# Kernel tuning notes

Hardware: AMD Instinct MI355X
Metric: run time of the kernel (lower is better)

The kernel has to match this reference:

```python
import jax, jax.numpy as jnp
import numpy as np

DOWNSAMPLING_K = 64  # number of pooled key/value positions


def setup_inputs() -> dict:
    key = jax.random.key(0)
    ks = jax.random.split(key, 8)
    B, S, H, N, D = 4, 4096, 1024, 16, 64
    s_in = 0.02  # glorot-like scale for H=1024 fan-in
    return {
        "query": jax.random.normal(ks[0], (B, S, H), jnp.float32),
        "key": jax.random.normal(ks[1], (B, S, H), jnp.float32),
        "value": jax.random.normal(ks[2], (B, S, H), jnp.float32),
        "Wq": jax.random.normal(ks[3], (H, N, D), jnp.float32) * s_in,
        "bq": jnp.zeros((N, D), jnp.float32),
        "Wk": jax.random.normal(ks[4], (H, N, D), jnp.float32) * s_in,
        "bk": jnp.zeros((N, D), jnp.float32),
        "Wv": jax.random.normal(ks[5], (H, N, D), jnp.float32) * s_in,
        "bv": jnp.zeros((N, D), jnp.float32),
        "Wo": jax.random.normal(ks[6], (N, D, H), jnp.float32) * s_in,
        "bo": jnp.zeros((H,), jnp.float32),
        "step": 0,
        "train": 0,
    }


def _downsample(x, k):
    # x: [B, S, N, D] -> mean-pool along sequence into k buckets -> [B, k, N, D]
    B, S, N, D = x.shape
    return x.reshape(B, k, S // k, N, D).mean(axis=2)


def reference(query, key, value, Wq, bq, Wk, bk, Wv, bv, Wo, bo, step, train):
    # QKV projections (DenseGeneral features=(num_heads, head_dim))
    q = jnp.einsum("bsh,hnd->bsnd", query, Wq) + bq  # [B,S,N,D]
    k = jnp.einsum("bsh,hnd->bsnd", key, Wk) + bk
    v = jnp.einsum("bsh,hnd->bsnd", value, Wv) + bv
    # Downsampled (sparse) attention: pool K,V to DOWNSAMPLING_K positions
    kd = _downsample(k, DOWNSAMPLING_K)  # [B,K,N,D]
    vd = _downsample(v, DOWNSAMPLING_K)
    scale = 1.0 / jnp.sqrt(jnp.asarray(q.shape[-1], q.dtype))
    scores = jnp.einsum("bsnd,bknd->bnsk", q, kd) * scale  # [B,N,S,K]
    attn = jax.nn.softmax(scores, axis=-1)
    a_v = jnp.einsum("bnsk,bknd->bsnd", attn, vd)  # [B,S,N,D]
    # Output projection (DenseGeneral over (-2,-1))
    out = jnp.einsum("bsnd,ndh->bsh", a_v, Wo) + bo  # [B,S,H]
    return out
```

## Files before the change

### kernel.cpp

```cpp
#include <hip/hip_runtime.h>

typedef unsigned short u16;
typedef unsigned int u32;
typedef __attribute__((ext_vector_type(8))) short bf16x8_t;
typedef __attribute__((ext_vector_type(4))) float f32x4_t;


#define MFMA_BF16 __builtin_amdgcn_mfma_f32_16x16x32_bf16

__device__ __forceinline__ u16 f2bf(float f) {
  union { float f; u32 u; } a; a.f = f;
  u32 u = a.u;
  u32 r = (u + 0x7FFFu + ((u >> 16) & 1u)) >> 16;
  return (u16)r;
}

__device__ __forceinline__ void async_load16(const void* g, void* l) {
  __builtin_amdgcn_global_load_lds(
      (const __attribute__((address_space(1))) void*)g,
      (__attribute__((address_space(3))) void*)l, 16, 0, 0);
}

__device__ __forceinline__ void stage64(const u16* __restrict__ src,
                                        char* lds_base, int t) {
  const int r = t >> 3;
  const int gch = (t & 7) ^ (r & 7);
  async_load16(src + (size_t)r * 1024 + gch * 8, lds_base + (t >> 6) * 1024);
}

__device__ __forceinline__ void acc4(float4& a, const float4 b) {
  a.x += b.x; a.y += b.y; a.z += b.z; a.w += b.w;
}

__global__ __launch_bounds__(512) void fused_stream(
    const float* __restrict__ query, const float* __restrict__ key,
    const float* __restrict__ value, const float* __restrict__ W0,
    const float* __restrict__ W1, const float* __restrict__ W2,
    const float* __restrict__ W3, u16* __restrict__ qcvt, u16* __restrict__ keyd,
    u16* __restrict__ valued, u16* __restrict__ T0, u16* __restrict__ T1,
    u16* __restrict__ T2, u16* __restrict__ T3) {
  __shared__ char smem[32768];
  const int z = blockIdx.x;
  const int t = threadIdx.x;
  if (z < 512) {
    float (*part)[256][4] = (float(*)[256][4])smem;
    const int bkk = z & 255;
    const float* x = (z >= 256) ? value : key;
    u16* xd = (z >= 256) ? valued : keyd;
    const int lane = t & 63, w = t >> 6;
    const float* base = x + (size_t)bkk * 65536 + (size_t)w * 8 * 1024;
#define LD4(j, s) (*(const float4*)(base + (size_t)(j) * 1024 + ((s) * 64 + lane) * 4))
    float4 a0 = {0.f, 0.f, 0.f, 0.f}, a1 = a0, a2 = a0, a3 = a0;
    float4 u0 = LD4(0, 0), u1 = LD4(0, 1), u2 = LD4(0, 2), u3 = LD4(0, 3);
    float4 u4 = LD4(1, 0), u5 = LD4(1, 1), u6 = LD4(1, 2), u7 = LD4(1, 3);
    float4 v0 = LD4(2, 0), v1 = LD4(2, 1), v2 = LD4(2, 2), v3 = LD4(2, 3);
    float4 v4 = LD4(3, 0), v5 = LD4(3, 1), v6 = LD4(3, 2), v7 = LD4(3, 3);
    acc4(a0, u0); acc4(a1, u1); acc4(a2, u2); acc4(a3, u3);
    acc4(a0, u4); acc4(a1, u5); acc4(a2, u6); acc4(a3, u7);
    u0 = LD4(4, 0); u1 = LD4(4, 1); u2 = LD4(4, 2); u3 = LD4(4, 3);
    u4 = LD4(5, 0); u5 = LD4(5, 1); u6 = LD4(5, 2); u7 = LD4(5, 3);
    acc4(a0, v0); acc4(a1, v1); acc4(a2, v2); acc4(a3, v3);
    acc4(a0, v4); acc4(a1, v5); acc4(a2, v6); acc4(a3, v7);
    v0 = LD4(6, 0); v1 = LD4(6, 1); v2 = LD4(6, 2); v3 = LD4(6, 3);
    v4 = LD4(7, 0); v5 = LD4(7, 1); v6 = LD4(7, 2); v7 = LD4(7, 3);
    acc4(a0, u0); acc4(a1, u1); acc4(a2, u2); acc4(a3, u3);
    acc4(a0, u4); acc4(a1, u5); acc4(a2, u6); acc4(a3, u7);
    acc4(a0, v0); acc4(a1, v1); acc4(a2, v2); acc4(a3, v3);
    acc4(a0, v4); acc4(a1, v5); acc4(a2, v6); acc4(a3, v7);
#undef LD4
    *(float4*)&part[w][0 * 64 + lane][0] = a0;
    *(float4*)&part[w][1 * 64 + lane][0] = a1;
    *(float4*)&part[w][2 * 64 + lane][0] = a2;
    *(float4*)&part[w][3 * 64 + lane][0] = a3;
    __syncthreads();
    if (t < 256) {
      float4 s = {0.f, 0.f, 0.f, 0.f};
#pragma unroll
      for (int w2 = 0; w2 < 8; ++w2) {
        const float4 v = *(const float4*)&part[w2][t][0];
        s.x += v.x; s.y += v.y; s.z += v.z; s.w += v.w;
      }
      ushort4 r;
      r.x = f2bf(s.x * 0.015625f);
      r.y = f2bf(s.y * 0.015625f);
      r.z = f2bf(s.z * 0.015625f);
      r.w = f2bf(s.w * 0.015625f);
      *(ushort4*)(xd + (size_t)bkk * 1024 + t * 4) = r;
    }
  } else if (z < 4608) {
    const size_t i = ((size_t)(z - 512) * 512 + t) * 8;
    const float4 a = *(const float4*)(query + i);
    const float4 b = *(const float4*)(query + i + 4);
    bf16x8_t o;
    o[0] = (short)f2bf(a.x); o[1] = (short)f2bf(a.y);
    o[2] = (short)f2bf(a.z); o[3] = (short)f2bf(a.w);
    o[4] = (short)f2bf(b.x); o[5] = (short)f2bf(b.y);
    o[6] = (short)f2bf(b.z); o[7] = (short)f2bf(b.w);
    *(bf16x8_t*)(qcvt + i) = o;
  } else {
    float (*tile)[65] = (float(*)[65])smem;
    const int blk = z - 4608;
    const int wsel = blk >> 8, tidx = blk & 255;
    const float* W = (wsel == 0) ? W0 : (wsel == 1) ? W1 : (wsel == 2) ? W2 : W3;
    u16* WT = (wsel == 0) ? T0 : (wsel == 1) ? T1 : (wsel == 2) ? T2 : T3;
    const int tr = (tidx >> 4) * 64;
    const int tc = (tidx & 15) * 64;
#pragma unroll
    for (int i = 0; i < 8; ++i) {
      int idx = i * 512 + t;
      int r = idx >> 6, c = idx & 63;
      tile[r][c] = W[(size_t)(tr + r) * 1024 + tc + c];
    }
    __syncthreads();
#pragma unroll
    for (int i = 0; i < 8; ++i) {
      int idx = i * 512 + t;
      int r = idx >> 6, c = idx & 63;
      WT[(size_t)(tc + r) * 1024 + tr + c] = f2bf(tile[c][r]);
    }
  }
}

__global__ __launch_bounds__(256) void gemm_kv(const u16* __restrict__ A0,
                                               const u16* __restrict__ A1,
                                               const u16* __restrict__ BT0,
                                               const u16* __restrict__ BT1,
                                               const float* __restrict__ bias0,
                                               const float* __restrict__ bias1,
                                               u16* __restrict__ C0,
                                               u16* __restrict__ C1) {
  constexpr int K = 1024, BK = 32;
  __shared__ u16 sA[128 * BK];
  __shared__ u16 sB[128 * BK];
  const int z = blockIdx.z;
  const u16* A = z ? A1 : A0;
  const u16* BT = z ? BT1 : BT0;
  const float* bias = z ? bias1 : bias0;
  u16* Cv = z ? C1 : C0;
  const int t = threadIdx.x;
  const int lane = t & 63;
  const int w = t >> 6;
  const int wr = w >> 1, wc = w & 1;
  const int m0 = blockIdx.x * 128;
  const int n0 = blockIdx.y * 128;
  const int c16 = lane & 15, r16 = lane >> 4;

  f32x4_t acc[4][4] = {};

  for (int k0 = 0; k0 < K; k0 += BK) {
#pragma unroll
    for (int i = 0; i < 2; ++i) {
      const int idx = i * 256 + t;
      const int row = idx >> 2, ch = idx & 3;
      const int gch = ch ^ ((row >> 1) & 3);
      async_load16(A + (size_t)(m0 + row) * K + k0 + gch * 8,
                   (char*)sA + (i * 256 + w * 64) * 16);
    }
#pragma unroll
    for (int i = 0; i < 2; ++i) {
      const int idx = i * 256 + t;
      const int row = idx >> 2, ch = idx & 3;
      const int gch = ch ^ ((row >> 1) & 3);
      async_load16(BT + (size_t)(n0 + row) * K + k0 + gch * 8,
                   (char*)sB + (i * 256 + w * 64) * 16);
    }
    __syncthreads();

    bf16x8_t af[4], bfv[4];
#pragma unroll
    for (int m = 0; m < 4; ++m) {
      const int ra = wr * 64 + m * 16 + c16;
      af[m] = *(const bf16x8_t*)&sA[ra * BK + ((r16 ^ ((ra >> 1) & 3)) << 3)];
    }
#pragma unroll
    for (int n = 0; n < 4; ++n) {
      const int rb = wc * 64 + n * 16 + c16;
      bfv[n] = *(const bf16x8_t*)&sB[rb * BK + ((r16 ^ ((rb >> 1) & 3)) << 3)];
    }
#pragma unroll
    for (int m = 0; m < 4; ++m)
#pragma unroll
      for (int n = 0; n < 4; ++n)
        acc[m][n] = MFMA_BF16(af[m], bfv[n], acc[m][n], 0, 0, 0);
    __syncthreads();
  }

#pragma unroll
  for (int m = 0; m < 4; ++m) {
    const int row0 = m0 + wr * 64 + m * 16 + r16 * 4;
#pragma unroll
    for (int n = 0; n < 4; ++n) {
      const int col = n0 + wc * 64 + n * 16 + c16;
      const float bvl = bias[col];
#pragma unroll
      for (int i = 0; i < 4; ++i) {
        const float val = acc[m][n][i] + bvl;
        if (z)
          Cv[(size_t)col * 256 + row0 + i] = f2bf(val);
        else
          Cv[(size_t)(row0 + i) * 1024 + col] = f2bf(val);
      }
    }
  }
}

#define GEMM256_KLOOP(A_, BT_)                                                          \
  const u16* Ab = (A_) + (size_t)bx * 256 * 1024;                                       \
  const u16* Bb = (BT_) + (size_t)by * 256 * 1024;                                      \
  stage64(Ab,                   lds,                 t);                                \
  stage64(Ab + 128 * 1024,      lds + 128 * 128,     t);                                \
  stage64(Bb,                   lds + 32768,         t);                                \
  stage64(Bb + 64 * 1024,       lds + 32768 + 8192,  t);                                \
  stage64(Bb + 128 * 1024,      lds + 32768 + 16384, t);                                \
  stage64(Bb + 192 * 1024,      lds + 32768 + 24576, t);                                \
  stage64(Ab + 64 * 1024,       lds + 64 * 128,      t);                                \
  stage64(Ab + 192 * 1024,      lds + 192 * 128,     t);                                \
  stage64(Ab + 64,              lds + 65536,         t);                                \
  stage64(Ab + 128 * 1024 + 64, lds + 65536 + 16384, t);                                \
  stage64(Bb + 64,              lds + 98304,         t);                                \
  stage64(Bb + 64 * 1024 + 64,  lds + 98304 + 8192,  t);                                \
  stage64(Bb + 128 * 1024 + 64, lds + 98304 + 16384, t);                                \
  stage64(Bb + 192 * 1024 + 64, lds + 98304 + 24576, t);                                \
  asm volatile("s_waitcnt vmcnt(6)" ::: "memory");                                      \
  __builtin_amdgcn_s_barrier();                                                         \
  for (int kt = 0; kt < 16; ++kt) {                                                     \
    const int slot = kt & 1;                                                            \
    const u16* sAs = (const u16*)(lds + slot * 65536);                                  \
    const u16* sBs = (const u16*)(lds + slot * 65536 + 32768);                          \
    char* sAn = lds + (slot ^ 1) * 65536;                                               \
    char* sAc = lds + slot * 65536;                                                     \
    char* sBc = lds + slot * 65536 + 32768;                                             \
    const int k1 = (kt < 15 ? kt + 1 : 15) * 64;                                        \
    const int k2 = (kt < 14 ? kt + 2 : 15) * 64;                                        \
    bf16x8_t af[4][2];                                                                  \
    _Pragma("unroll") for (int m = 0; m < 4; ++m) {                                     \
      const int row = wm * 128 + m * 16 + c16;                                          \
      _Pragma("unroll") for (int kk = 0; kk < 2; ++kk)                                  \
        af[m][kk] = *(const bf16x8_t*)&sAs[row * 64 + (((kk * 4 + r16) ^ c7) << 3)];    \
    }                                                                                   \
    _Pragma("unroll") for (int n = 0; n < 2; ++n) {                                     \
      const int row = wn * 64 + n * 16 + c16;                                           \
      _Pragma("unroll") for (int kk = 0; kk < 2; ++kk)                                  \
        bfr[n][kk] = *(const bf16x8_t*)&sBs[row * 64 + (((kk * 4 + r16) ^ c7) << 3)];   \
    }                                                                                   \
    stage64(Ab + (size_t)64 * 1024 + k1,  sAn + 64 * 128,  t);                          \
    stage64(Ab + (size_t)192 * 1024 + k1, sAn + 192 * 128, t);                          \
    asm volatile("" ::: "memory");                                                      \
    __builtin_amdgcn_s_barrier();                                                       \
    asm volatile("s_waitcnt lgkmcnt(0)" ::: "memory");                                  \
    __builtin_amdgcn_sched_barrier(0);                                                  \
    __builtin_amdgcn_s_setprio(1);                                                      \
    _Pragma("unroll") for (int m = 0; m < 4; ++m)                                       \
      _Pragma("unroll") for (int n = 0; n < 2; ++n)                                     \
        _Pragma("unroll") for (int kk = 0; kk < 2; ++kk)                                \
          acc[m][n] = MFMA_BF16(af[m][kk], bfr[n][kk], acc[m][n], 0, 0, 0);             \
    __builtin_amdgcn_s_setprio(0);                                                      \
    asm volatile("" ::: "memory");                                                      \
    __builtin_amdgcn_s_barrier();                                                       \
    _Pragma("unroll") for (int n = 2; n < 4; ++n) {                                     \
      const int row = wn * 64 + n * 16 + c16;                                           \
      _Pragma("unroll") for (int kk = 0; kk < 2; ++kk)                                  \
        bfr[n][kk] = *(const bf16x8_t*)&sBs[row * 64 + (((kk * 4 + r16) ^ c7) << 3)];   \
    }                                                                                   \
    stage64(Ab + k2,                      sAc,             t);                          \
    stage64(Ab + (size_t)128 * 1024 + k2, sAc + 128 * 128, t);                          \
    asm volatile("" ::: "memory");                                                      \
    __builtin_amdgcn_s_barrier();                                                       \
    asm volatile("s_waitcnt lgkmcnt(0)" ::: "memory");                                  \
    __builtin_amdgcn_sched_barrier(0);                                                  \
    __builtin_amdgcn_s_setprio(1);                                                      \
    _Pragma("unroll") for (int m = 0; m < 4; ++m)                                       \
      _Pragma("unroll") for (int n = 2; n < 4; ++n)                                     \
        _Pragma("unroll") for (int kk = 0; kk < 2; ++kk)                                \
          acc[m][n] = MFMA_BF16(af[m][kk], bfr[n][kk], acc[m][n], 0, 0, 0);             \
    __builtin_amdgcn_s_setprio(0);                                                      \
    asm volatile("s_waitcnt vmcnt(10)" ::: "memory");                                   \
    __builtin_amdgcn_s_barrier();                                                       \
    _Pragma("unroll") for (int m = 0; m < 4; ++m) {                                     \
      const int row = wm * 128 + 64 + m * 16 + c16;                                     \
      _Pragma("unroll") for (int kk = 0; kk < 2; ++kk)                                  \
        af[m][kk] = *(const bf16x8_t*)&sAs[row * 64 + (((kk * 4 + r16) ^ c7) << 3)];    \
    }                                                                                   \
    stage64(Bb + k2,                     sBc,        t);                                \
    stage64(Bb + (size_t)64 * 1024 + k2, sBc + 8192, t);                                \
    asm volatile("" ::: "memory");                                                      \
    __builtin_amdgcn_s_barrier();                                                       \
    asm volatile("s_waitcnt lgkmcnt(0)" ::: "memory");                                  \
    __builtin_amdgcn_sched_barrier(0);                                                  \
    __builtin_amdgcn_s_setprio(1);                                                      \
    _Pragma("unroll") for (int m = 0; m < 4; ++m)                                       \
      _Pragma("unroll") for (int n = 0; n < 2; ++n)                                     \
        _Pragma("unroll") for (int kk = 0; kk < 2; ++kk)                                \
          acc[4 + m][n] = MFMA_BF16(af[m][kk], bfr[n][kk], acc[4 + m][n], 0, 0, 0);     \
    __builtin_amdgcn_s_setprio(0);                                                      \
    asm volatile("" ::: "memory");                                                      \
    __builtin_amdgcn_s_barrier();                                                       \
    stage64(Bb + (size_t)128 * 1024 + k2, sBc + 16384, t);                              \
    stage64(Bb + (size_t)192 * 1024 + k2, sBc + 24576, t);                              \
    asm volatile("" ::: "memory");                                                      \
    __builtin_amdgcn_s_barrier();                                                       \
    __builtin_amdgcn_sched_barrier(0);                                                  \
    __builtin_amdgcn_s_setprio(1);                                                      \
    _Pragma("unroll") for (int m = 0; m < 4; ++m)                                       \
      _Pragma("unroll") for (int n = 2; n < 4; ++n)                                     \
        _Pragma("unroll") for (int kk = 0; kk < 2; ++kk)                                \
          acc[4 + m][n] = MFMA_BF16(af[m][kk], bfr[n][kk], acc[4 + m][n], 0, 0, 0);     \
    __builtin_amdgcn_s_setprio(0);                                                      \
    asm volatile("s_waitcnt vmcnt(8)" ::: "memory");                                    \
    __builtin_amdgcn_s_barrier();                                                       \
  }

template <bool C_BF16>
__global__ __launch_bounds__(512) void gemm256(const u16* __restrict__ A,
                                               const u16* __restrict__ BT,
                                               const float* __restrict__ bias,
                                               void* __restrict__ Cv) {
  __shared__ u16 sAB[65536];
  char* lds = (char*)sAB;
  const int t = threadIdx.x;
  const int lane = t & 63;
  const int w = t >> 6;
  const int wm = w >> 2, wn = w & 3;
  const int c16 = lane & 15, r16 = lane >> 4, c7 = c16 & 7;
  const int tile = (blockIdx.x & 7) * 32 + (blockIdx.x >> 3);
  const int bx = tile >> 2, by = tile & 3;
  f32x4_t acc[8][4] = {};
  bf16x8_t bfr[4][2];
  GEMM256_KLOOP(A, BT)
#pragma unroll
  for (int m = 0; m < 8; ++m) {
    const int grow = bx * 256 + wm * 128 + m * 16 + r16 * 4;
#pragma unroll
    for (int n = 0; n < 4; ++n) {
      const int col = by * 256 + wn * 64 + n * 16 + c16;
      const float bvl = bias[col];
#pragma unroll
      for (int i = 0; i < 4; ++i) {
        const float val = acc[m][n][i] + bvl;
        if constexpr (C_BF16)
          ((u16*)Cv)[(size_t)(grow + i) * 1024 + col] = f2bf(val);
        else
          ((float*)Cv)[(size_t)(grow + i) * 1024 + col] = val;
      }
    }
  }
}

#define ATTN_EPI_HALF(HALF)                                                              \
  {                                                                                      \
    asm volatile("s_waitcnt lgkmcnt(0)" ::: "memory");                                   \
    _Pragma("unroll") for (int m = 0; m < 4; ++m)                                        \
      _Pragma("unroll") for (int nq = 0; nq < 4; ++nq) {                                 \
        const int d = nq * 16 + c16;                                                     \
        const float bvl = bias[n_head * 64 + d];                                         \
        _Pragma("unroll") for (int i = 0; i < 4; ++i) {                                  \
          const int row = m * 16 + r16 * 4 + i;                                          \
          qh[(row * 128 + ((d * 2) ^ ((row & 7) << 4))) >> 1] =                          \
              f2bf(acc[HALF * 4 + m][nq][i] + bvl);                                      \
        }                                                                                \
      }                                                                                  \
    if (HALF == 0) {                                                                     \
      asm volatile("s_waitcnt vmcnt(0) lgkmcnt(0)" ::: "memory");                        \
      __builtin_amdgcn_s_barrier();                                                      \
    } else {                                                                             \
      asm volatile("s_waitcnt lgkmcnt(0)" ::: "memory");                                 \
    }                                                                                    \
    bf16x8_t aq[4][2];                                                                   \
    _Pragma("unroll") for (int st = 0; st < 4; ++st) {                                   \
      const int row = st * 16 + c16;                                                     \
      const int rsw = (row & 7) << 4;                                                    \
      _Pragma("unroll") for (int dt = 0; dt < 2; ++dt)                                   \
        aq[st][dt] =                                                                     \
            *(const bf16x8_t*)&qh[(row * 128 + ((dt * 64 + r16 * 16) ^ rsw)) >> 1];      \
    }                                                                                    \
    asm volatile("s_waitcnt lgkmcnt(0)" ::: "memory");                                   \
    __builtin_amdgcn_sched_barrier(0);                                                   \
    u16* sP = qh;                                                                        \
    _Pragma("unroll") for (int st = 0; st < 4; ++st) {                                   \
      f32x4_t accs[4];                                                                   \
      _Pragma("unroll") for (int nn = 0; nn < 4; ++nn) {                                 \
        const u16* kr = &kdw[(nn * 16 + c16) * 64];                                      \
        bf16x8_t b0 = *(const bf16x8_t*)&kr[((r16 * 16) ^ swz) >> 1];                    \
        bf16x8_t b1 = *(const bf16x8_t*)&kr[((64 + r16 * 16) ^ swz) >> 1];               \
        f32x4_t a = {0.f, 0.f, 0.f, 0.f};                                                \
        a = MFMA_BF16(aq[st][0], b0, a, 0, 0, 0);                                        \
        a = MFMA_BF16(aq[st][1], b1, a, 0, 0, 0);                                        \
        accs[nn] = a;                                                                    \
      }                                                                                  \
      float ex[4][4], rs[4];                                                             \
      _Pragma("unroll") for (int i = 0; i < 4; ++i) {                                    \
        float mx = fmaxf(fmaxf(accs[0][i], accs[1][i]), fmaxf(accs[2][i], accs[3][i]));  \
        _Pragma("unroll") for (int off = 1; off < 16; off <<= 1)                         \
          mx = fmaxf(mx, __shfl_xor(mx, off));                                           \
        mx *= 0.125f;                                                                    \
        float s = 0.f;                                                                   \
        _Pragma("unroll") for (int nn = 0; nn < 4; ++nn) {                               \
          float e = __expf(accs[nn][i] * 0.125f - mx);                                   \
          ex[nn][i] = e;                                                                 \
          s += e;                                                                        \
        }                                                                                \
        _Pragma("unroll") for (int off = 1; off < 16; off <<= 1)                         \
          s += __shfl_xor(s, off);                                                       \
        rs[i] = 1.f / s;                                                                 \
      }                                                                                  \
      _Pragma("unroll") for (int i = 0; i < 4; ++i) {                                    \
        const int row = r16 * 4 + i;                                                     \
        const int rsw = (row & 7) << 4;                                                  \
        _Pragma("unroll") for (int nn = 0; nn < 4; ++nn)                                 \
          sP[row * 64 + (((nn * 32 + c16 * 2) ^ rsw) >> 1)] = f2bf(ex[nn][i]);           \
      }                                                                                  \
      asm volatile("s_waitcnt lgkmcnt(0)" ::: "memory");                                 \
      bf16x8_t pa0 = *(const bf16x8_t*)&sP[c16 * 64 + (((r16 * 16) ^ swz) >> 1)];        \
      bf16x8_t pa1 = *(const bf16x8_t*)&sP[c16 * 64 + (((64 + r16 * 16) ^ swz) >> 1)];   \
      f32x4_t accv[4];                                                                   \
      _Pragma("unroll") for (int dt = 0; dt < 4; ++dt) {                                 \
        const u16* vr = &vdw[(dt * 16 + c16) * 64];                                      \
        bf16x8_t v0 = *(const bf16x8_t*)&vr[((r16 * 16) ^ swz) >> 1];                    \
        bf16x8_t v1 = *(const bf16x8_t*)&vr[((64 + r16 * 16) ^ swz) >> 1];               \
        f32x4_t a = {0.f, 0.f, 0.f, 0.f};                                                \
        a = MFMA_BF16(pa0, v0, a, 0, 0, 0);                                              \
        a = MFMA_BF16(pa1, v1, a, 0, 0, 0);                                              \
        accv[dt] = a;                                                                    \
      }                                                                                  \
      _Pragma("unroll") for (int i = 0; i < 4; ++i) {                                    \
        const int row = r16 * 4 + i;                                                     \
        const int rsw = (row & 7) << 4;                                                  \
        _Pragma("unroll") for (int dt = 0; dt < 4; ++dt)                                 \
          sP[row * 64 + (((dt * 32 + c16 * 2) ^ rsw) >> 1)] = f2bf(accv[dt][i] * rs[i]); \
      }                                                                                  \
      asm volatile("s_waitcnt lgkmcnt(0)" ::: "memory");                                 \
      const int srow_base = b * 4096 + s0b + wm * 128 + HALF * 64 + st * 16;             \
      _Pragma("unroll") for (int r = 0; r < 2; ++r) {                                    \
        const int row = r * 8 + (lane >> 3);                                             \
        const int cb = ((lane & 7) * 16) ^ ((row & 7) << 4);                             \
        bf16x8_t vv = *(const bf16x8_t*)&sP[row * 64 + (cb >> 1)];                       \
        *(bf16x8_t*)(av + (size_t)(srow_base + row) * 1024 + n_head * 64 +               \
                     (lane & 7) * 8) = vv;                                               \
      }                                                                                  \
    }                                                                                    \
  }

__global__ __launch_bounds__(512) void gemm256_attn(const u16* __restrict__ A,
                                                    const u16* __restrict__ BT,
                                                    const float* __restrict__ bias,
                                                    const u16* __restrict__ kdb,
                                                    const u16* __restrict__ vdTb,
                                                    u16* __restrict__ av) {
  __shared__ u16 sAB[65536];
  char* lds = (char*)sAB;
  const int t = threadIdx.x;
  const int lane = t & 63;
  const int w = t >> 6;
  const int wm = w >> 2, wn = w & 3;
  const int c16 = lane & 15, r16 = lane >> 4, c7 = c16 & 7;
  const int tile = (blockIdx.x & 7) * 32 + (blockIdx.x >> 3);
  const int bx = tile >> 2, by = tile & 3;
  f32x4_t acc[8][4] = {};
  bf16x8_t bfr[4][2];
  GEMM256_KLOOP(A, BT)

  asm volatile("s_waitcnt vmcnt(0)" ::: "memory");
  __builtin_amdgcn_s_barrier();

  const int b = bx >> 4;
  const int s0b = (bx & 15) * 256;
  char* kdL = lds + 65536;
  char* vdL = lds + 65536 + 32768;
  {
    const int kk = t >> 3;
    const int colb = ((t & 7) ^ (kk & 7)) << 4;
#pragma unroll
    for (int h = 0; h < 4; ++h) {
      const int n = by * 4 + h;
      async_load16((const char*)kdb + (size_t)(b * 64 + kk) * 2048 + n * 128 + colb,
                   kdL + h * 8192 + (t >> 6) * 1024);
      async_load16((const char*)vdTb + (size_t)(n * 64 + kk) * 512 + b * 128 + colb,
                   vdL + h * 8192 + (t >> 6) * 1024);
    }
  }
  u16* qh = (u16*)(lds + w * 8192);
  const int n_head = by * 4 + wn;
  const u16* kdw = (const u16*)(kdL + wn * 8192);
  const u16* vdw = (const u16*)(vdL + wn * 8192);
  const int swz = (c16 & 7) << 4;

  ATTN_EPI_HALF(0)
  ATTN_EPI_HALF(1)
}

extern "C" void kernel_launch(void* const* d_in, const int* in_sizes, int n_in,
                              void* d_out, int out_size, void* d_ws, size_t ws_size,
                              hipStream_t stream) {
  (void)in_sizes; (void)n_in; (void)out_size; (void)ws_size;
  const float* query = (const float*)d_in[0];
  const float* key   = (const float*)d_in[1];
  const float* value = (const float*)d_in[2];
  const float* Wq = (const float*)d_in[3];
  const float* bq = (const float*)d_in[4];
  const float* Wk = (const float*)d_in[5];
  const float* bk = (const float*)d_in[6];
  const float* Wv = (const float*)d_in[7];
  const float* bv = (const float*)d_in[8];
  const float* Wo = (const float*)d_in[9];
  const float* bo = (const float*)d_in[10];
  float* out = (float*)d_out;

  char* ws = (char*)d_ws;
  const size_t MB = 1024 * 1024;
  u16* WqT    = (u16*)(ws + 0 * MB);
  u16* WkT    = (u16*)(ws + 2 * MB);
  u16* WvT    = (u16*)(ws + 4 * MB);
  u16* WoT    = (u16*)(ws + 6 * MB);
  u16* keyd   = (u16*)(ws + 8 * MB);
  u16* valued = (u16*)(ws + 8 * MB + 512 * 1024);
  u16* kdb    = (u16*)(ws + 9 * MB);
  u16* vdTb   = (u16*)(ws + 9 * MB + 512 * 1024);
  u16* avb    = (u16*)(ws + 10 * MB);
  u16* qcvt   = (u16*)((char*)d_out + 32 * MB);

  fused_stream<<<5632, 512, 0, stream>>>(query, key, value, Wq, Wk, Wv, Wo,
                                         qcvt, keyd, valued, WqT, WkT, WvT, WoT);

  gemm_kv<<<dim3(2, 8, 2), 256, 0, stream>>>(keyd, valued, WkT, WvT, bk, bv, kdb, vdTb);

  gemm256_attn<<<256, 512, 0, stream>>>(qcvt, WqT, bq, kdb, vdTb, avb);
  gemm256<false><<<256, 512, 0, stream>>>(avb, WoT, bo, out);
}
```

Baseline: 159.7 us.

## Fuse query bf16 conversion into Q-projection GEMM k-loop

Removes the standalone pass that converted the fp32 query to bf16 in global memory. The Q-projection/attention GEMM now loads fp32 query rows into registers, converts them and writes swizzled bf16 into LDS within its double-buffered k-loop, while B tiles are still staged asynchronously. This avoids writing and re-reading the converted query buffer, in exchange for more VGPR pressure, conversion ALU work inside the MFMA loop, and fp32 A reads repeated across column tiles.

```diff
diff --git a/kernel.cpp b/kernel.cpp
--- a/kernel.cpp
+++ b/kernel.cpp
@@ -32,13 +32,29 @@
   a.x += b.x; a.y += b.y; a.z += b.z; a.w += b.w;
 }
 
+__device__ __forceinline__ void cvt_write_row(const float4 a0, const float4 a1,
+                                              const float4 a2, const float4 a3,
+                                              int row, int q4, char* base) {
+  bf16x8_t c0, c1;
+  c0[0] = (short)f2bf(a0.x); c0[1] = (short)f2bf(a0.y);
+  c0[2] = (short)f2bf(a0.z); c0[3] = (short)f2bf(a0.w);
+  c0[4] = (short)f2bf(a1.x); c0[5] = (short)f2bf(a1.y);
+  c0[6] = (short)f2bf(a1.z); c0[7] = (short)f2bf(a1.w);
+  c1[0] = (short)f2bf(a2.x); c1[1] = (short)f2bf(a2.y);
+  c1[2] = (short)f2bf(a2.z); c1[3] = (short)f2bf(a2.w);
+  c1[4] = (short)f2bf(a3.x); c1[5] = (short)f2bf(a3.y);
+  c1[6] = (short)f2bf(a3.z); c1[7] = (short)f2bf(a3.w);
+  const int sw = row & 7;
+  *(bf16x8_t*)(base + (size_t)row * 128 + (((2 * q4) ^ sw) << 4)) = c0;
+  *(bf16x8_t*)(base + (size_t)row * 128 + (((2 * q4 + 1) ^ sw) << 4)) = c1;
+}
+
 __global__ __launch_bounds__(512) void fused_stream(
-    const float* __restrict__ query, const float* __restrict__ key,
-    const float* __restrict__ value, const float* __restrict__ W0,
-    const float* __restrict__ W1, const float* __restrict__ W2,
-    const float* __restrict__ W3, u16* __restrict__ qcvt, u16* __restrict__ keyd,
-    u16* __restrict__ valued, u16* __restrict__ T0, u16* __restrict__ T1,
-    u16* __restrict__ T2, u16* __restrict__ T3) {
+    const float* __restrict__ key, const float* __restrict__ value,
+    const float* __restrict__ W0, const float* __restrict__ W1,
+    const float* __restrict__ W2, const float* __restrict__ W3,
+    u16* __restrict__ keyd, u16* __restrict__ valued, u16* __restrict__ T0,
+    u16* __restrict__ T1, u16* __restrict__ T2, u16* __restrict__ T3) {
   __shared__ char smem[32768];
   const int z = blockIdx.x;
   const int t = threadIdx.x;
@@ -87,19 +103,9 @@
       r.w = f2bf(s.w * 0.015625f);
       *(ushort4*)(xd + (size_t)bkk * 1024 + t * 4) = r;
     }
-  } else if (z < 4608) {
-    const size_t i = ((size_t)(z - 512) * 512 + t) * 8;
-    const float4 a = *(const float4*)(query + i);
-    const float4 b = *(const float4*)(query + i + 4);
-    bf16x8_t o;
-    o[0] = (short)f2bf(a.x); o[1] = (short)f2bf(a.y);
-    o[2] = (short)f2bf(a.z); o[3] = (short)f2bf(a.w);
-    o[4] = (short)f2bf(b.x); o[5] = (short)f2bf(b.y);
-    o[6] = (short)f2bf(b.z); o[7] = (short)f2bf(b.w);
-    *(bf16x8_t*)(qcvt + i) = o;
   } else {
     float (*tile)[65] = (float(*)[65])smem;
-    const int blk = z - 4608;
+    const int blk = z - 512;
     const int wsel = blk >> 8, tidx = blk & 255;
     const float* W = (wsel == 0) ? W0 : (wsel == 1) ? W1 : (wsel == 2) ? W2 : W3;
     u16* WT = (wsel == 0) ? T0 : (wsel == 1) ? T1 : (wsel == 2) ? T2 : T3;
@@ -307,6 +313,129 @@
           acc[4 + m][n] = MFMA_BF16(af[m][kk], bfr[n][kk], acc[4 + m][n], 0, 0, 0);     \
     __builtin_amdgcn_s_setprio(0);                                                      \
     asm volatile("s_waitcnt vmcnt(8)" ::: "memory");                                    \
+    __builtin_amdgcn_s_barrier();                                                       \
+  }
+
+#define GEMM256_KLOOP_F32A(AF_, BT_)                                                    \
+  const float* Af = (AF_) + (size_t)bx * 256 * 1024;                                    \
+  const u16* Bb = (BT_) + (size_t)by * 256 * 1024;                                      \
+  {                                                                                     \
+                                                  \
+    float4 x0 = LDA4(arow01, 0, 0), x1 = LDA4(arow01, 0, 1);                            \
+    float4 x2 = LDA4(arow01, 0, 2), x3 = LDA4(arow01, 0, 3);                            \
+    float4 y0 = LDA4(arow23, 0, 0), y1 = LDA4(arow23, 0, 1);                            \
+    float4 y2 = LDA4(arow23, 0, 2), y3 = LDA4(arow23, 0, 3);                            \
+    float4 z0 = LDA4(arow01, 64, 0), z1 = LDA4(arow01, 64, 1);                          \
+    float4 z2 = LDA4(arow01, 64, 2), z3 = LDA4(arow01, 64, 3);                          \
+    cvt_write_row(x0, x1, x2, x3, arow01, q4, lds);                                     \
+    cvt_write_row(y0, y1, y2, y3, arow23, q4, lds);                                     \
+    cvt_write_row(z0, z1, z2, z3, arow01, q4, lds + 65536);                             \
+  }                                                                                     \
+  stage64(Bb,                  lds + 32768,         t);                                 \
+  stage64(Bb + 64 * 1024,      lds + 32768 + 8192,  t);                                 \
+  stage64(Bb + 128 * 1024,     lds + 32768 + 16384, t);                                 \
+  stage64(Bb + 192 * 1024,     lds + 32768 + 24576, t);                                 \
+  asm volatile("" ::: "memory");                                                        \
+  stage64(Bb + 64,              lds + 98304,         t);                                \
+  stage64(Bb + 64 * 1024 + 64,  lds + 98304 + 8192,  t);                                \
+  stage64(Bb + 128 * 1024 + 64, lds + 98304 + 16384, t);                                \
+  stage64(Bb + 192 * 1024 + 64, lds + 98304 + 24576, t);                                \
+  ra0 = LDA4(arow23, 64, 0); ra1 = LDA4(arow23, 64, 1);                                 \
+  ra2 = LDA4(arow23, 64, 2); ra3 = LDA4(arow23, 64, 3);                                 \
+  rb0 = LDA4(arow01, 128, 0); rb1 = LDA4(arow01, 128, 1);                               \
+  rb2 = LDA4(arow01, 128, 2); rb3 = LDA4(arow01, 128, 3);                               \
+  asm volatile("s_waitcnt lgkmcnt(0)" ::: "memory");                                    \
+  asm volatile("s_waitcnt vmcnt(12)" ::: "memory");      \
+  __builtin_amdgcn_s_barrier();                                                         \
+  for (int kt = 0; kt < 16; ++kt) {                                                     \
+    const int slot = kt & 1;                                                            \
+    const u16* sAs = (const u16*)(lds + slot * 65536);                                  \
+    const u16* sBs = (const u16*)(lds + slot * 65536 + 32768);                          \
+    char* sAn = lds + (slot ^ 1) * 65536;                                               \
+    char* sAc = lds + slot * 65536;                                                     \
+    char* sBc = lds + slot * 65536 + 32768;                                             \
+    const int rowN = arow23;                                      \
+    const int k2 = (kt < 14 ? kt + 2 : 15) * 64;                                        \
+    const int k3 = (kt < 13 ? kt + 3 : 15) * 64;                                        \
+    bf16x8_t af[4][2];                                                                  \
+                                                                 \
+    _Pragma("unroll") for (int m = 0; m < 4; ++m) {                                     \
+      const int row = wm * 128 + m * 16 + c16;                                          \
+      _Pragma("unroll") for (int kk = 0; kk < 2; ++kk)                                  \
+        af[m][kk] = *(const bf16x8_t*)&sAs[row * 64 + (((kk * 4 + r16) ^ c7) << 3)];    \
+    }                                                                                   \
+    _Pragma("unroll") for (int n = 0; n < 2; ++n) {                                     \
+      const int row = wn * 64 + n * 16 + c16;                                           \
+      _Pragma("unroll") for (int kk = 0; kk < 2; ++kk)                                  \
+        bfr[n][kk] = *(const bf16x8_t*)&sBs[row * 64 + (((kk * 4 + r16) ^ c7) << 3)];   \
+    }                                                                                   \
+    cvt_write_row(ra0, ra1, ra2, ra3, rowN, q4, sAn);                   \
+    asm volatile("s_waitcnt lgkmcnt(0)" ::: "memory");   \
+    __builtin_amdgcn_s_barrier();                                                       \
+    __builtin_amdgcn_sched_barrier(0);                                                  \
+    __builtin_amdgcn_s_setprio(1);                                                      \
+    _Pragma("unroll") for (int m = 0; m < 4; ++m)                                       \
+      _Pragma("unroll") for (int n = 0; n < 2; ++n)                                     \
+        _Pragma("unroll") for (int kk = 0; kk < 2; ++kk)                                \
+          acc[m][n] = MFMA_BF16(af[m][kk], bfr[n][kk], acc[m][n], 0, 0, 0);             \
+    __builtin_amdgcn_s_setprio(0);                                                      \
+    asm volatile("" ::: "memory");                                                      \
+    __builtin_amdgcn_s_barrier();                                                       \
+                                                                 \
+    _Pragma("unroll") for (int n = 2; n < 4; ++n) {                                     \
+      const int row = wn * 64 + n * 16 + c16;                                           \
+      _Pragma("unroll") for (int kk = 0; kk < 2; ++kk)                                  \
+        bfr[n][kk] = *(const bf16x8_t*)&sBs[row * 64 + (((kk * 4 + r16) ^ c7) << 3)];   \
+    }                                                                                   \
+    cvt_write_row(rb0, rb1, rb2, rb3, arow01, q4, sAc);                 \
+    asm volatile("s_waitcnt lgkmcnt(0)" ::: "memory");                                  \
+    __builtin_amdgcn_s_barrier();                                                       \
+    __builtin_amdgcn_sched_barrier(0);                                                  \
+    __builtin_amdgcn_s_setprio(1);                                                      \
+    _Pragma("unroll") for (int m = 0; m < 4; ++m)                                       \
+      _Pragma("unroll") for (int n = 2; n < 4; ++n)                                     \
+        _Pragma("unroll") for (int kk = 0; kk < 2; ++kk)                                \
+          acc[m][n] = MFMA_BF16(af[m][kk], bfr[n][kk], acc[m][n], 0, 0, 0);             \
+    __builtin_amdgcn_s_setprio(0);                                                      \
+    asm volatile("" ::: "memory");                                                      \
+    __builtin_amdgcn_s_barrier();                                                       \
+                                                                 \
+    _Pragma("unroll") for (int m = 0; m < 4; ++m) {                                     \
+      const int row = wm * 128 + 64 + m * 16 + c16;                                     \
+      _Pragma("unroll") for (int kk = 0; kk < 2; ++kk)                                  \
+        af[m][kk] = *(const bf16x8_t*)&sAs[row * 64 + (((kk * 4 + r16) ^ c7) << 3)];    \
+    }                                                                                   \
+    stage64(Bb + k2,                     sBc,        t);                                \
+    stage64(Bb + (size_t)64 * 1024 + k2, sBc + 8192, t);                                \
+    ra0 = LDA4(arow23, k2, 0); ra1 = LDA4(arow23, k2, 1);                               \
+    ra2 = LDA4(arow23, k2, 2); ra3 = LDA4(arow23, k2, 3);                               \
+    asm volatile("" ::: "memory");                                                      \
+    __builtin_amdgcn_s_barrier();                                                       \
+    asm volatile("s_waitcnt lgkmcnt(0)" ::: "memory");                                  \
+    __builtin_amdgcn_sched_barrier(0);                                                  \
+    __builtin_amdgcn_s_setprio(1);                                                      \
+    _Pragma("unroll") for (int m = 0; m < 4; ++m)                                       \
+      _Pragma("unroll") for (int n = 0; n < 2; ++n)                                     \
+        _Pragma("unroll") for (int kk = 0; kk < 2; ++kk)                                \
+          acc[4 + m][n] = MFMA_BF16(af[m][kk], bfr[n][kk], acc[4 + m][n], 0, 0, 0);     \
+    __builtin_amdgcn_s_setprio(0);                                                      \
+    asm volatile("" ::: "memory");                                                      \
+    __builtin_amdgcn_s_barrier();                                                       \
+                                                                 \
+    stage64(Bb + (size_t)128 * 1024 + k2, sBc + 16384, t);                              \
+    stage64(Bb + (size_t)192 * 1024 + k2, sBc + 24576, t);                              \
+    rb0 = LDA4(arow01, k3, 0); rb1 = LDA4(arow01, k3, 1);                               \
+    rb2 = LDA4(arow01, k3, 2); rb3 = LDA4(arow01, k3, 3);                               \
+    asm volatile("" ::: "memory");                                                      \
+    __builtin_amdgcn_s_barrier();                                                       \
+    __builtin_amdgcn_sched_barrier(0);                                                  \
+    __builtin_amdgcn_s_setprio(1);                                                      \
+    _Pragma("unroll") for (int m = 0; m < 4; ++m)                                       \
+      _Pragma("unroll") for (int n = 2; n < 4; ++n)                                     \
+        _Pragma("unroll") for (int kk = 0; kk < 2; ++kk)                                \
+          acc[4 + m][n] = MFMA_BF16(af[m][kk], bfr[n][kk], acc[4 + m][n], 0, 0, 0);     \
+    __builtin_amdgcn_s_setprio(0);                                                      \
+    asm volatile("" ::: "memory");                                                      \
     __builtin_amdgcn_s_barrier();                                                       \
   }
 
@@ -440,7 +569,7 @@
     }                                                                                    \
   }
 
-__global__ __launch_bounds__(512) void gemm256_attn(const u16* __restrict__ A,
+__global__ __launch_bounds__(512) void gemm256_attn(const float* __restrict__ Aq,
                                                     const u16* __restrict__ BT,
                                                     const float* __restrict__ bias,
                                                     const u16* __restrict__ kdb,
@@ -455,11 +584,19 @@
   const int c16 = lane & 15, r16 = lane >> 4, c7 = c16 & 7;
   const int tile = (blockIdx.x & 7) * 32 + (blockIdx.x >> 3);
   const int bx = tile >> 2, by = tile & 3;
+  const int ar = t >> 2;
+  const int q4 = t & 3;
+  const int arow01 = (ar < 64) ? ar : 64 + ar;
+  const int arow23 = arow01 + 64;
+#define LDA4(row, koff, j) \
+  (*(const float4*)(Af + (size_t)(row) * 1024 + (koff) + q4 * 16 + (j) * 4))
+  float4 ra0, ra1, ra2, ra3, rb0, rb1, rb2, rb3;
   f32x4_t acc[8][4] = {};
   bf16x8_t bfr[4][2];
-  GEMM256_KLOOP(A, BT)
-
-  asm volatile("s_waitcnt vmcnt(0)" ::: "memory");
+  GEMM256_KLOOP_F32A(Aq, BT)
+#undef LDA4
+
+  asm volatile("s_waitcnt vmcnt(0) lgkmcnt(0)" ::: "memory");
   __builtin_amdgcn_s_barrier();
 
   const int b = bx >> 4;
@@ -516,13 +653,12 @@
   u16* kdb    = (u16*)(ws + 9 * MB);
   u16* vdTb   = (u16*)(ws + 9 * MB + 512 * 1024);
   u16* avb    = (u16*)(ws + 10 * MB);
-  u16* qcvt   = (u16*)((char*)d_out + 32 * MB);
-
-  fused_stream<<<5632, 512, 0, stream>>>(query, key, value, Wq, Wk, Wv, Wo,
-                                         qcvt, keyd, valued, WqT, WkT, WvT, WoT);
+
+  fused_stream<<<1536, 512, 0, stream>>>(key, value, Wq, Wk, Wv, Wo,
+                                         keyd, valued, WqT, WkT, WvT, WoT);
 
   gemm_kv<<<dim3(2, 8, 2), 256, 0, stream>>>(keyd, valued, WkT, WvT, bk, bv, kdb, vdTb);
 
-  gemm256_attn<<<256, 512, 0, stream>>>(qcvt, WqT, bq, kdb, vdTb, avb);
+  gemm256_attn<<<256, 512, 0, stream>>>(query, WqT, bq, kdb, vdTb, avb);
   gemm256<false><<<256, 512, 0, stream>>>(avb, WoT, bo, out);
 }
```

Result: slower. 175.3 us (+9.8%).
